# Optimization experiments

Hardware: AMD Instinct MI355X
Metric: run time of the kernel (lower is better)

Reference implementation:

```python
import jax, jax.numpy as jnp
import numpy as np

CONV = 332.07156


def setup_inputs() -> dict:
    key = jax.random.key(0)
    ks = jax.random.split(key, 6)
    B, N, C = 4, 2048, 32
    X = jax.random.normal(ks[0], (B, N, 3), dtype=jnp.float32) * 5.0
    embs = jax.random.uniform(ks[1], (B, N, C), dtype=jnp.float32)
    qs = jax.random.normal(ks[2], (B, N), dtype=jnp.float32)
    paired_mask = jnp.zeros((B, N, N), dtype=bool)
    # learned parameters, initialized as in the torch module
    Born_factor = jax.random.normal(ks[3], (C,), dtype=jnp.float32) * 0.1 + 1.0
    die_factor = jax.random.normal(ks[4], (C,), dtype=jnp.float32) * 0.1 + 4.0
    screening_filter = jax.random.normal(ks[5], (2 * C + 1, 1), dtype=jnp.float32) * 0.1
    screening_filter = screening_filter.at[-1, :].set(1.0)
    return {"X": X, "embs": embs, "qs": qs, "paired_mask": paired_mask,
            "Born_factor": Born_factor, "die_factor": die_factor,
            "screening_filter": screening_filter}


def reference(X, embs, qs, paired_mask, Born_factor, die_factor, screening_filter):
    B, N, _ = X.shape
    C = embs.shape[-1]
    # all-pairs displacement and distance; note +1e-6 added per component before sum
    V = X[:, None, :, :] - X[:, :, None, :]            # (B,N,N,3)
    D = jnp.sqrt(jnp.sum(V * V + 1e-6, axis=-1))       # (B,N,N)
    invD = 1.0 / (D + 1e-6)
    # per-atom Born / dielectric scalars
    atomic_die = embs @ die_factor + 1e-6               # (B,N)
    R = embs @ Born_factor + 1.0                        # (B,N)
    E_self = -(1.0 - 1.0 / atomic_die) * qs / (R + 1e-6)  # (B,N)
    # pairwise screening: cat([emb_i, emb_j, D]) @ filter, algebraically separable
    w_i = screening_filter[:C, 0]                       # (C,)
    w_j = screening_filter[C:2 * C, 0]                  # (C,)
    w_d = screening_filter[2 * C, 0]                    # scalar
    s_i = embs @ w_i                                    # (B,N)
    s_j = embs @ w_j                                    # (B,N)
    screening = s_i[:, :, None] + s_j[:, None, :] + w_d * D  # (B,N,N)
    E_pair = invD * screening                           # (B,N,N)
    Etotal = CONV * (E_self.sum(axis=1) + 0.5 * E_pair.sum(axis=(1, 2))) * 0.01
    Etotal = jnp.where(jnp.isnan(Etotal), jnp.float32(1e-6), Etotal)
    return Etotal
```

## Files before the change

### kernel.cpp

```cpp
#include <hip/hip_runtime.h>
#include <math.h>

#define NB 4
#define NA 2048
#define NC 32
#define NATOM (NB * NA)
#define IT 256
#define UI 2
#define ITILE (IT * UI)
#define NS 64
#define JT (NA / NS)
#define NI (NA / ITILE)

static constexpr float CONV001 = 3.3207156f;

#define WS_PI   0
#define WS_PJ   32768
#define WS_PAIR 65536
#define WS_SELF 66560

__global__ void __launch_bounds__(256)
atom_kernel(const float* __restrict__ X,
            const float* __restrict__ embs,
            const float* __restrict__ qs,
            const float* __restrict__ born,
            const float* __restrict__ die,
            const float* __restrict__ sf,
            float* __restrict__ ws) {
    const int a = blockIdx.x * 256 + threadIdx.x;
    const float4* e4 = (const float4*)(embs + (size_t)a * NC);

    float si = 0.f, sj = 0.f, ad = 0.f, R = 0.f;
    #pragma unroll
    for (int c = 0; c < NC / 4; ++c) {
        float4 ev = e4[c];
        si = fmaf(ev.x, sf[4 * c + 0], fmaf(ev.y, sf[4 * c + 1],
             fmaf(ev.z, sf[4 * c + 2], fmaf(ev.w, sf[4 * c + 3], si))));
        sj = fmaf(ev.x, sf[NC + 4 * c + 0], fmaf(ev.y, sf[NC + 4 * c + 1],
             fmaf(ev.z, sf[NC + 4 * c + 2], fmaf(ev.w, sf[NC + 4 * c + 3], sj))));
        ad = fmaf(ev.x, die[4 * c + 0], fmaf(ev.y, die[4 * c + 1],
             fmaf(ev.z, die[4 * c + 2], fmaf(ev.w, die[4 * c + 3], ad))));
        R  = fmaf(ev.x, born[4 * c + 0], fmaf(ev.y, born[4 * c + 1],
             fmaf(ev.z, born[4 * c + 2], fmaf(ev.w, born[4 * c + 3], R))));
    }
    float x = X[a * 3 + 0];
    float y = X[a * 3 + 1];
    float z = X[a * 3 + 2];
    float4* Pi = (float4*)(ws + WS_PI);
    float4* Pj = (float4*)(ws + WS_PJ);
    Pi[a] = make_float4(x, y, z, si);
    Pj[a] = make_float4(x, y, z, sj);

    ad += 1e-6f;
    R  += 1.0f;
    float eself = -(1.0f - __builtin_amdgcn_rcpf(ad)) * qs[a]
                  * __builtin_amdgcn_rcpf(R + 1e-6f);

    #pragma unroll
    for (int off = 32; off > 0; off >>= 1)
        eself += __shfl_down(eself, off, 64);
    __shared__ float wsum[4];
    int lane = threadIdx.x & 63;
    int w = threadIdx.x >> 6;
    if (lane == 0) wsum[w] = eself;
    __syncthreads();
    if (threadIdx.x == 0)
        ws[WS_SELF + blockIdx.x] = wsum[0] + wsum[1] + wsum[2] + wsum[3];
}

__global__ void __launch_bounds__(IT)
pair_kernel(const float* __restrict__ wsc,
            float* __restrict__ ws) {
    const int b  = blockIdx.z;
    const int t  = threadIdx.x;
    const int i0 = b * NA + blockIdx.y * ITILE;
    const int j0 = b * NA + blockIdx.x * JT;

    const float4* Pi = (const float4*)(wsc + WS_PI);
    const float4* Pj = (const float4*)(wsc + WS_PJ);

    __shared__ float4 jd[JT];
    if (t < JT)
        jd[t] = Pj[j0 + t];

    float4 id[UI];
    #pragma unroll
    for (int u = 0; u < UI; ++u)
        id[u] = Pi[i0 + u * IT + t];
    __syncthreads();

    float acc[UI] = {0.f, 0.f};
    #pragma unroll 4
    for (int jj = 0; jj < JT; ++jj) {
        float4 v = jd[jj];
        #pragma unroll
        for (int u = 0; u < UI; ++u) {
            float dx = v.x - id[u].x;
            float dy = v.y - id[u].y;
            float dz = v.z - id[u].z;
            float d2 = fmaf(dx, dx, fmaf(dy, dy, fmaf(dz, dz, 3e-6f)));
            acc[u] = fmaf(__builtin_amdgcn_rsqf(d2), id[u].w + v.w, acc[u]);
        }
    }

    float a = acc[0] + acc[1];
    #pragma unroll
    for (int off = 32; off > 0; off >>= 1)
        a += __shfl_down(a, off, 64);
    __shared__ float wsum[IT / 64];
    int lane = t & 63;
    int w = t >> 6;
    if (lane == 0) wsum[w] = a;
    __syncthreads();
    if (t == 0) {
        int slot = (b * NI + blockIdx.y) * NS + blockIdx.x;
        ws[WS_PAIR + slot] = wsum[0] + wsum[1] + wsum[2] + wsum[3];
    }
}

__global__ void __launch_bounds__(1024)
finalize_kernel(const float* __restrict__ ws,
                const float* __restrict__ sf,
                float* __restrict__ out) {
    int t = threadIdx.x;
    float v = ws[WS_PAIR + t];
    #pragma unroll
    for (int off = 32; off > 0; off >>= 1)
        v += __shfl_down(v, off, 64);
    __shared__ float wsum[16];
    if ((t & 63) == 0) wsum[t >> 6] = v;
    __syncthreads();
    if (t < NB) {
        float pair = wsum[4 * t] + wsum[4 * t + 1]
                   + wsum[4 * t + 2] + wsum[4 * t + 3];
        float self = 0.f;
        #pragma unroll
        for (int k = 0; k < 8; ++k)
            self += ws[WS_SELF + t * 8 + k];
        float wd = sf[2 * NC];
        float r = CONV001 * 0.5f * (pair + 2.0f * self
                                    + wd * (float)NA * (float)NA);
        out[t] = isnan(r) ? 1e-6f : r;
    }
}

extern "C" void kernel_launch(void* const* d_in, const int* in_sizes, int n_in,
                              void* d_out, int out_size, void* d_ws, size_t ws_size,
                              hipStream_t stream) {
    const float* X    = (const float*)d_in[0];
    const float* embs = (const float*)d_in[1];
    const float* qs   = (const float*)d_in[2];
    const float* born = (const float*)d_in[4];
    const float* die  = (const float*)d_in[5];
    const float* sf   = (const float*)d_in[6];
    float* ws  = (float*)d_ws;
    float* out = (float*)d_out;

    atom_kernel<<<NATOM / 256, 256, 0, stream>>>(X, embs, qs, born, die, sf, ws);
    pair_kernel<<<dim3(NS, NI, NB), IT, 0, stream>>>(ws, ws);
    finalize_kernel<<<1, 1024, 0, stream>>>(ws, sf, out);
}
```

Before: 109.4 us.

## Fuse atom, pair and finalize kernels into one with last-block reduction

Merges the per-atom projection, pairwise sum and final reduction into a single launch. Each pair block recomputes the s_i/s_j projections for its own atoms from embs instead of reading precomputed float4s. The self-energy is computed by the s==0 blocks, and the last block to finish, detected through an atomic counter, performs the final reduction. This removes two kernel launches and the inter-kernel gaps, at the cost of redundant embedding dot products in every block and atomic synchronisation overhead.

```diff
diff --git a/kernel.cpp b/kernel.cpp
--- a/kernel.cpp
+++ b/kernel.cpp
@@ -4,89 +4,71 @@
 #define NB 4
 #define NA 2048
 #define NC 32
-#define NATOM (NB * NA)
 #define IT 256
 #define UI 2
 #define ITILE (IT * UI)
 #define NS 64
 #define JT (NA / NS)
 #define NI (NA / ITILE)
+#define NBLK (NS * NI * NB)
 
 static constexpr float CONV001 = 3.3207156f;
 
-#define WS_PI   0
-#define WS_PJ   32768
-#define WS_PAIR 65536
-#define WS_SELF 66560
+#define WS_PAIR 0
+#define WS_SELF NBLK
 
-__global__ void __launch_bounds__(256)
-atom_kernel(const float* __restrict__ X,
-            const float* __restrict__ embs,
-            const float* __restrict__ qs,
-            const float* __restrict__ born,
-            const float* __restrict__ die,
-            const float* __restrict__ sf,
-            float* __restrict__ ws) {
-    const int a = blockIdx.x * 256 + threadIdx.x;
-    const float4* e4 = (const float4*)(embs + (size_t)a * NC);
-
-    float si = 0.f, sj = 0.f, ad = 0.f, R = 0.f;
-    #pragma unroll
-    for (int c = 0; c < NC / 4; ++c) {
-        float4 ev = e4[c];
-        si = fmaf(ev.x, sf[4 * c + 0], fmaf(ev.y, sf[4 * c + 1],
-             fmaf(ev.z, sf[4 * c + 2], fmaf(ev.w, sf[4 * c + 3], si))));
-        sj = fmaf(ev.x, sf[NC + 4 * c + 0], fmaf(ev.y, sf[NC + 4 * c + 1],
-             fmaf(ev.z, sf[NC + 4 * c + 2], fmaf(ev.w, sf[NC + 4 * c + 3], sj))));
-        ad = fmaf(ev.x, die[4 * c + 0], fmaf(ev.y, die[4 * c + 1],
-             fmaf(ev.z, die[4 * c + 2], fmaf(ev.w, die[4 * c + 3], ad))));
-        R  = fmaf(ev.x, born[4 * c + 0], fmaf(ev.y, born[4 * c + 1],
-             fmaf(ev.z, born[4 * c + 2], fmaf(ev.w, born[4 * c + 3], R))));
-    }
-    float x = X[a * 3 + 0];
-    float y = X[a * 3 + 1];
-    float z = X[a * 3 + 2];
-    float4* Pi = (float4*)(ws + WS_PI);
-    float4* Pj = (float4*)(ws + WS_PJ);
-    Pi[a] = make_float4(x, y, z, si);
-    Pj[a] = make_float4(x, y, z, sj);
-
-    ad += 1e-6f;
-    R  += 1.0f;
-    float eself = -(1.0f - __builtin_amdgcn_rcpf(ad)) * qs[a]
-                  * __builtin_amdgcn_rcpf(R + 1e-6f);
-
-    #pragma unroll
-    for (int off = 32; off > 0; off >>= 1)
-        eself += __shfl_down(eself, off, 64);
-    __shared__ float wsum[4];
-    int lane = threadIdx.x & 63;
-    int w = threadIdx.x >> 6;
-    if (lane == 0) wsum[w] = eself;
-    __syncthreads();
-    if (threadIdx.x == 0)
-        ws[WS_SELF + blockIdx.x] = wsum[0] + wsum[1] + wsum[2] + wsum[3];
-}
+__device__ int g_counter = 0;
 
 __global__ void __launch_bounds__(IT)
-pair_kernel(const float* __restrict__ wsc,
-            float* __restrict__ ws) {
+fused_kernel(const float* __restrict__ X,
+             const float* __restrict__ embs,
+             const float* __restrict__ qs,
+             const float* __restrict__ born,
+             const float* __restrict__ die,
+             const float* __restrict__ sf,
+             float* __restrict__ ws,
+             float* __restrict__ out) {
+    const int t  = threadIdx.x;
+    const int s  = blockIdx.x;
+    const int y  = blockIdx.y;
     const int b  = blockIdx.z;
-    const int t  = threadIdx.x;
-    const int i0 = b * NA + blockIdx.y * ITILE;
-    const int j0 = b * NA + blockIdx.x * JT;
-
-    const float4* Pi = (const float4*)(wsc + WS_PI);
-    const float4* Pj = (const float4*)(wsc + WS_PJ);
+    const int i0 = b * NA + y * ITILE;
+    const int j0 = b * NA + s * JT;
+    const int lane = t & 63;
+    const int w    = t >> 6;
 
     __shared__ float4 jd[JT];
-    if (t < JT)
-        jd[t] = Pj[j0 + t];
+    __shared__ float  wsum[IT / 64];
+    __shared__ float  ssum[IT / 64];
+    __shared__ int    lastflag;
+
+    if (t < JT) {
+        const int a = j0 + t;
+        const float4* e4 = (const float4*)(embs + (size_t)a * NC);
+        float sj = 0.f;
+        #pragma unroll
+        for (int c = 0; c < NC / 4; ++c) {
+            float4 ev = e4[c];
+            sj = fmaf(ev.x, sf[NC + 4 * c + 0], fmaf(ev.y, sf[NC + 4 * c + 1],
+                 fmaf(ev.z, sf[NC + 4 * c + 2], fmaf(ev.w, sf[NC + 4 * c + 3], sj))));
+        }
+        jd[t] = make_float4(X[a * 3 + 0], X[a * 3 + 1], X[a * 3 + 2], sj);
+    }
 
     float4 id[UI];
     #pragma unroll
-    for (int u = 0; u < UI; ++u)
-        id[u] = Pi[i0 + u * IT + t];
+    for (int u = 0; u < UI; ++u) {
+        const int a = i0 + u * IT + t;
+        const float4* e4 = (const float4*)(embs + (size_t)a * NC);
+        float si = 0.f;
+        #pragma unroll
+        for (int c = 0; c < NC / 4; ++c) {
+            float4 ev = e4[c];
+            si = fmaf(ev.x, sf[4 * c + 0], fmaf(ev.y, sf[4 * c + 1],
+                 fmaf(ev.z, sf[4 * c + 2], fmaf(ev.w, sf[4 * c + 3], si))));
+        }
+        id[u] = make_float4(X[a * 3 + 0], X[a * 3 + 1], X[a * 3 + 2], si);
+    }
     __syncthreads();
 
     float acc[UI] = {0.f, 0.f};
@@ -103,44 +85,76 @@
         }
     }
 
-    float a = acc[0] + acc[1];
+    float pa = acc[0] + acc[1];
     #pragma unroll
     for (int off = 32; off > 0; off >>= 1)
-        a += __shfl_down(a, off, 64);
-    __shared__ float wsum[IT / 64];
-    int lane = t & 63;
-    int w = t >> 6;
-    if (lane == 0) wsum[w] = a;
+        pa += __shfl_down(pa, off, 64);
+    if (lane == 0) wsum[w] = pa;
+
+    if (s == 0) {
+        float eself = 0.f;
+        #pragma unroll
+        for (int u = 0; u < UI; ++u) {
+            const int a = i0 + u * IT + t;
+            const float4* e4 = (const float4*)(embs + (size_t)a * NC);
+            float ad = 0.f, R = 0.f;
+            #pragma unroll
+            for (int c = 0; c < NC / 4; ++c) {
+                float4 ev = e4[c];
+                ad = fmaf(ev.x, die[4 * c + 0], fmaf(ev.y, die[4 * c + 1],
+                     fmaf(ev.z, die[4 * c + 2], fmaf(ev.w, die[4 * c + 3], ad))));
+                R  = fmaf(ev.x, born[4 * c + 0], fmaf(ev.y, born[4 * c + 1],
+                     fmaf(ev.z, born[4 * c + 2], fmaf(ev.w, born[4 * c + 3], R))));
+            }
+            ad += 1e-6f;
+            R  += 1.0f;
+            eself += -(1.0f - __builtin_amdgcn_rcpf(ad)) * qs[a]
+                     * __builtin_amdgcn_rcpf(R + 1e-6f);
+        }
+        #pragma unroll
+        for (int off = 32; off > 0; off >>= 1)
+            eself += __shfl_down(eself, off, 64);
+        if (lane == 0) ssum[w] = eself;
+    }
     __syncthreads();
+
     if (t == 0) {
-        int slot = (b * NI + blockIdx.y) * NS + blockIdx.x;
-        ws[WS_PAIR + slot] = wsum[0] + wsum[1] + wsum[2] + wsum[3];
+        const int slot = (b * NI + y) * NS + s;
+        __hip_atomic_store(&ws[WS_PAIR + slot],
+                           wsum[0] + wsum[1] + wsum[2] + wsum[3],
+                           __ATOMIC_RELEASE, __HIP_MEMORY_SCOPE_AGENT);
+        if (s == 0)
+            __hip_atomic_store(&ws[WS_SELF + b * NI + y],
+                               ssum[0] + ssum[1] + ssum[2] + ssum[3],
+                               __ATOMIC_RELEASE, __HIP_MEMORY_SCOPE_AGENT);
+        int old = __hip_atomic_fetch_add(&g_counter, 1,
+                                         __ATOMIC_ACQ_REL, __HIP_MEMORY_SCOPE_AGENT);
+        lastflag = (old == NBLK - 1);
     }
-}
+    __syncthreads();
+    if (!lastflag) return;
 
-__global__ void __launch_bounds__(1024)
-finalize_kernel(const float* __restrict__ ws,
-                const float* __restrict__ sf,
-                float* __restrict__ out) {
-    int t = threadIdx.x;
-    float v = ws[WS_PAIR + t];
-    #pragma unroll
-    for (int off = 32; off > 0; off >>= 1)
-        v += __shfl_down(v, off, 64);
-    __shared__ float wsum[16];
-    if ((t & 63) == 0) wsum[t >> 6] = v;
-    __syncthreads();
-    if (t < NB) {
-        float pair = wsum[4 * t] + wsum[4 * t + 1]
-                   + wsum[4 * t + 2] + wsum[4 * t + 3];
-        float self = 0.f;
+    {
+        const int bb = w;
+        float v = 0.f;
         #pragma unroll
-        for (int k = 0; k < 8; ++k)
-            self += ws[WS_SELF + t * 8 + k];
-        float wd = sf[2 * NC];
-        float r = CONV001 * 0.5f * (pair + 2.0f * self
-                                    + wd * (float)NA * (float)NA);
-        out[t] = isnan(r) ? 1e-6f : r;
+        for (int k = 0; k < 4; ++k)
+            v += __hip_atomic_load(&ws[WS_PAIR + bb * (NI * NS) + k * 64 + lane],
+                                   __ATOMIC_ACQUIRE, __HIP_MEMORY_SCOPE_AGENT);
+        if (lane < NI)
+            v += 2.0f * __hip_atomic_load(&ws[WS_SELF + bb * NI + lane],
+                                          __ATOMIC_ACQUIRE, __HIP_MEMORY_SCOPE_AGENT);
+        #pragma unroll
+        for (int off = 32; off > 0; off >>= 1)
+            v += __shfl_down(v, off, 64);
+        if (lane == 0) {
+            const float wd = sf[2 * NC];
+            float r = CONV001 * 0.5f * (v + wd * (float)NA * (float)NA);
+            out[bb] = isnan(r) ? 1e-6f : r;
+        }
+        if (t == 0)
+            __hip_atomic_store(&g_counter, 0,
+                               __ATOMIC_RELAXED, __HIP_MEMORY_SCOPE_AGENT);
     }
 }
 
@@ -153,10 +167,7 @@
     const float* born = (const float*)d_in[4];
     const float* die  = (const float*)d_in[5];
     const float* sf   = (const float*)d_in[6];
-    float* ws  = (float*)d_ws;
-    float* out = (float*)d_out;
 
-    atom_kernel<<<NATOM / 256, 256, 0, stream>>>(X, embs, qs, born, die, sf, ws);
-    pair_kernel<<<dim3(NS, NI, NB), IT, 0, stream>>>(ws, ws);
-    finalize_kernel<<<1, 1024, 0, stream>>>(ws, sf, out);
+    fused_kernel<<<dim3(NS, NI, NB), IT, 0, stream>>>(
+        X, embs, qs, born, die, sf, (float*)d_ws, (float*)d_out);
 }
```

Result: slower. 145.0 us (+32.6%).
